# Optimization experiments

Measured on AMD Instinct MI355X. Metric: run time of the kernel, lower is better.

## Reference

```python
import jax, jax.numpy as jnp
import numpy as np

D_MODEL = 1024
HIDDEN = 2048
D_STATE = 16
KERN = 3
BATCH = 2
SEQ = 2048


def _layernorm(x, g, b, eps=1e-5):
    m = jnp.mean(x, axis=-1, keepdims=True)
    v = jnp.var(x, axis=-1, keepdims=True)
    return (x - m) * jax.lax.rsqrt(v + eps) * g + b


def setup_inputs() -> dict:
    key = jax.random.key(0)
    ks = jax.random.split(key, 10)
    w_scale = 0.02  # keep pre-activations in a sane range (mimics trained-net init)
    return {
        "x": jax.random.normal(ks[0], (BATCH, SEQ, D_MODEL), jnp.float32),
        "W_x": jax.random.normal(ks[1], (HIDDEN, D_MODEL), jnp.float32) * w_scale,
        "b_x": jnp.zeros((HIDDEN,), jnp.float32),
        "W_g": jax.random.normal(ks[2], (HIDDEN, D_MODEL), jnp.float32) * w_scale,
        "b_g": jnp.zeros((HIDDEN,), jnp.float32),
        "conv_w": jax.random.normal(ks[3], (HIDDEN, 1, KERN), jnp.float32) * 0.3,
        "conv_b": jnp.zeros((HIDDEN,), jnp.float32),
        "A_raw": jax.random.normal(ks[4], (HIDDEN, D_STATE), jnp.float32),
        "B_ssm": jax.random.normal(ks[5], (HIDDEN, D_STATE), jnp.float32),
        "C_ssm": jax.random.normal(ks[6], (HIDDEN, D_STATE), jnp.float32),
        "W_dt": jax.random.normal(ks[7], (HIDDEN, D_MODEL), jnp.float32) * w_scale,
        "b_dt": jnp.zeros((HIDDEN,), jnp.float32),
        "W_out": jax.random.normal(ks[8], (D_MODEL, HIDDEN), jnp.float32) * w_scale,
        "b_out": jnp.zeros((D_MODEL,), jnp.float32),
        "ln_g": jnp.ones((D_MODEL,), jnp.float32),
        "ln_b": jnp.zeros((D_MODEL,), jnp.float32),
    }


def reference(x, W_x, b_x, W_g, b_g, conv_w, conv_b, A_raw, B_ssm, C_ssm,
              W_dt, b_dt, W_out, b_out, ln_g, ln_b):
    # projections: u, gate
    u = jnp.einsum('bld,hd->blh', x, W_x) + b_x                    # [B,L,H]
    g = jax.nn.sigmoid(jnp.einsum('bld,hd->blh', x, W_g) + b_g)    # [B,L,H]
    # depthwise conv over time (padding = kernel//2, 'same' for odd kernel)
    pad = conv_w.shape[-1] // 2
    h = jax.lax.conv_general_dilated(
        jnp.transpose(u, (0, 2, 1)), conv_w,
        window_strides=(1,), padding=[(pad, pad)],
        feature_group_count=conv_w.shape[0],
        dimension_numbers=('NCH', 'OIH', 'NCH')) + conv_b[None, :, None]
    h = jnp.transpose(h, (0, 2, 1))                                # [B,L,H]
    u = u * g + h * (1.0 - g)
    # time-invariant dt per channel (mean over batch & time, clamped)
    dt = jax.nn.softplus(jnp.einsum('bld,hd->blh', x, W_dt) + b_dt).mean(axis=(0, 1))
    dt = jnp.clip(dt, 1e-3, 2.0)                                   # [H]
    # discretize
    A = -jax.nn.softplus(A_raw)                                    # [H,S]
    A_d = jnp.exp(A * dt[:, None])                                 # [H,S]
    B_d = (A_d - 1.0) / (A + 1e-6) * B_ssm                         # [H,S]
    # selective scan: state s[b,h,k] = A_d*s + B_d*u_t ; y = <s, C>
    Bsz, L, H = u.shape
    S = A_d.shape[1]

    def step(carry, u_t):                                          # u_t: [B,H]
        new = A_d[None] * carry + B_d[None] * u_t[:, :, None]      # [B,H,S]
        y_t = jnp.einsum('bhs,hs->bh', new, C_ssm)
        return new, y_t

    init = jnp.zeros((Bsz, H, S), dtype=u.dtype)
    _, ys = jax.lax.scan(step, init, jnp.transpose(u, (1, 0, 2)))  # ys: [L,B,H]
    y = jnp.transpose(ys, (1, 0, 2))                               # [B,L,H]
    out = jnp.einsum('blh,dh->bld', y, W_out) + b_out
    return _layernorm(x + out, ln_g, ln_b)
```

## Files before the change

kernel.cpp:

```cpp
#include <hip/hip_runtime.h>
#include <math.h>

#define D_MODEL 1024
#define HIDDEN  2048
#define D_STATE 16
#define BATCH   2
#define SEQ     2048
#define NTOK    (BATCH*SEQ)
#define CHUNK   64
#define NCHUNK  (SEQ/CHUNK)

typedef __attribute__((ext_vector_type(8))) short bf16x8;
typedef __attribute__((ext_vector_type(8))) unsigned short ushort8;
typedef __attribute__((ext_vector_type(4))) float f32x4;

#define GLOAD_LDS16(gptr, lptr) \
    __builtin_amdgcn_global_load_lds((const __attribute__((address_space(1))) void*)(gptr), \
                                     (__attribute__((address_space(3))) void*)(lptr), 16, 0, 0)

__device__ __forceinline__ float softplus_f(float x) {
    return fmaxf(x, 0.0f) + log1pf(expf(-fabsf(x)));
}
__device__ __forceinline__ float sigmoid_f(float x) {
    return 1.0f / (1.0f + expf(-x));
}
__device__ __forceinline__ ushort f2bf(float f) {
    unsigned u = __float_as_uint(f);
    unsigned r = (u + 0x7fffu + ((u >> 16) & 1u)) >> 16;
    return (ushort)r;
}
__device__ __forceinline__ float bf2f(ushort u) {
    return __uint_as_float(((unsigned)u) << 16);
}

__global__ __launch_bounds__(256) void cvt_all(
    const float* __restrict__ x, const float* __restrict__ Wx,
    const float* __restrict__ Wg, const float* __restrict__ Wdt,
    const float* __restrict__ Wout, ushort* __restrict__ arena)
{
    int i = blockIdx.x * 256 + threadIdx.x;
    const float* src; int base;
    if      (i < 1048576) { src = x;    base = 0; }
    else if (i < 1572864) { src = Wx;   base = 1048576; }
    else if (i < 2097152) { src = Wg;   base = 1572864; }
    else if (i < 2621440) { src = Wdt;  base = 2097152; }
    else                  { src = Wout; base = 2621440; }
    float4 v = reinterpret_cast<const float4*>(src)[i - base];
    ushort4 o = { f2bf(v.x), f2bf(v.y), f2bf(v.z), f2bf(v.w) };
    reinterpret_cast<ushort4*>(arena)[i] = o;
}

__device__ __forceinline__ void kloop_pipe3(
    const ushort* __restrict__ A, const ushort* __restrict__ B,
    int K, int m0, int n0, ushort* As, ushort* Bs,
    f32x4 (&acc)[4][4], int lane, int w, int wm, int wn)
{
    const int lr   = lane >> 2;
    const int qsrc = (lane & 3) ^ ((lane >> 3) & 3);
    const int kc   = qsrc * 8;
    const int quad = lane >> 4;
    const int fr   = lane & 15;
    const int chq  = quad ^ ((fr >> 1) & 3);

    const int slab0 = w * 2;
    const int r0 = slab0 * 16 + lr;
    const int r1 = r0 + 16;
    const size_t ga0 = (size_t)(m0 + r0) * K + kc;
    const size_t ga1 = (size_t)(m0 + r1) * K + kc;
    const size_t gb0 = (size_t)(n0 + r0) * K + kc;
    const size_t gb1 = (size_t)(n0 + r1) * K + kc;

    const int niter = K / 32;
    GLOAD_LDS16(A + ga0,      &As[slab0 * 512]);
    GLOAD_LDS16(A + ga1,      &As[slab0 * 512 + 512]);
    GLOAD_LDS16(B + gb0,      &Bs[slab0 * 512]);
    GLOAD_LDS16(B + gb1,      &Bs[slab0 * 512 + 512]);
    GLOAD_LDS16(A + ga0 + 32, &As[4096 + slab0 * 512]);
    GLOAD_LDS16(A + ga1 + 32, &As[4096 + slab0 * 512 + 512]);
    GLOAD_LDS16(B + gb0 + 32, &Bs[4096 + slab0 * 512]);
    GLOAD_LDS16(B + gb1 + 32, &Bs[4096 + slab0 * 512 + 512]);

    int buf = 0;
    for (int i = 0; i < niter; i++) {
        asm volatile("s_waitcnt vmcnt(4) lgkmcnt(0)" ::: "memory");
        asm volatile("s_barrier" ::: "memory");
        int nb = buf + 2; if (nb >= 3) nb -= 3;
        const size_t koff = (i + 2 < niter) ? (size_t)(i + 2) * 32 : 0;
        GLOAD_LDS16(A + ga0 + koff, &As[nb * 4096 + slab0 * 512]);
        GLOAD_LDS16(A + ga1 + koff, &As[nb * 4096 + slab0 * 512 + 512]);
        GLOAD_LDS16(B + gb0 + koff, &Bs[nb * 4096 + slab0 * 512]);
        GLOAD_LDS16(B + gb1 + koff, &Bs[nb * 4096 + slab0 * 512 + 512]);

        const ushort* as = &As[buf * 4096];
        const ushort* bs = &Bs[buf * 4096];
        bf16x8 af[4], bfv[4];
        #pragma unroll
        for (int t = 0; t < 4; t++) {
            af[t]  = *reinterpret_cast<const bf16x8*>(&as[(wm * 64 + t * 16 + fr) * 32 + chq * 8]);
            bfv[t] = *reinterpret_cast<const bf16x8*>(&bs[(wn * 64 + t * 16 + fr) * 32 + chq * 8]);
        }
        #pragma unroll
        for (int ii = 0; ii < 4; ii++)
            #pragma unroll
            for (int jj = 0; jj < 4; jj++)
                acc[ii][jj] = __builtin_amdgcn_mfma_f32_16x16x32_bf16(af[ii], bfv[jj], acc[ii][jj], 0, 0, 0);
        buf = (buf == 2) ? 0 : buf + 1;
    }
    asm volatile("s_waitcnt vmcnt(0) lgkmcnt(0)" ::: "memory");
    asm volatile("s_barrier" ::: "memory");
}

__global__ __launch_bounds__(256) void proj_gemm_fused(
    const ushort* __restrict__ xbf, const ushort* __restrict__ Wcat,
    const float* __restrict__ b_x, const float* __restrict__ b_g,
    const float* __restrict__ b_dt, ushort* __restrict__ u_out,
    ushort* __restrict__ g_out, float* __restrict__ dt_sum)
{
    __shared__ ushort S[24576];
    ushort* As = S;
    ushort* Bs = S + 12288;
    const int tid = threadIdx.x, lane = tid & 63, w = tid >> 6;
    const int wm = w & 1, wn = w >> 1;
    const int m0 = blockIdx.x * 128, n0 = blockIdx.y * 128;
    const int quad = lane >> 4, fr = lane & 15;

    f32x4 acc[4][4];
    #pragma unroll
    for (int i = 0; i < 4; i++)
        #pragma unroll
        for (int j = 0; j < 4; j++)
            acc[i][j] = (f32x4){0.f, 0.f, 0.f, 0.f};

    kloop_pipe3(xbf, Wcat, D_MODEL, m0, n0, As, Bs, acc, lane, w, wm, wn);

    const int region = n0 >> 11;
    const int ncb = n0 & 2047;

    if (region == 2) {
        #pragma unroll
        for (int j = 0; j < 4; j++) {
            int n = ncb + wn * 64 + j * 16 + fr;
            float bj = b_dt[n];
            float s = 0.f;
            #pragma unroll
            for (int i = 0; i < 4; i++)
                #pragma unroll
                for (int r = 0; r < 4; r++)
                    s += softplus_f(acc[i][j][r] + bj);
            s += __shfl_xor(s, 16);
            s += __shfl_xor(s, 32);
            if (lane < 16) atomicAdd(&dt_sum[n], s);
        }
    } else {
        const float* bias = region ? b_g : b_x;
        ushort* out = region ? g_out : u_out;
        ushort* Cs = S;
        #pragma unroll
        for (int j = 0; j < 4; j++) {
            int col = wn * 64 + j * 16 + fr;
            float bj = bias[ncb + col];
            #pragma unroll
            for (int i = 0; i < 4; i++) {
                int row = wm * 64 + i * 16 + quad * 4;
                #pragma unroll
                for (int r = 0; r < 4; r++) {
                    float v = acc[i][j][r] + bj;
                    if (region) v = sigmoid_f(v);
                    Cs[(row + r) * 128 + col] = f2bf(v);
                }
            }
        }
        __syncthreads();
        #pragma unroll
        for (int k = 0; k < 8; k++) {
            int v = k * 256 + tid;
            int row = v >> 4, c = (v & 15) * 8;
            *reinterpret_cast<ushort8*>(&out[(size_t)(m0 + row) * HIDDEN + ncb + c]) =
                *reinterpret_cast<const ushort8*>(&Cs[v * 8]);
        }
    }
}

__global__ __launch_bounds__(256) void gemm_out64(
    const ushort* __restrict__ ybf, const ushort* __restrict__ Wout,
    const float* __restrict__ b_out, const float* __restrict__ x,
    float* __restrict__ resid)
{
    __shared__ ushort S[18432];
    ushort* As = S;
    ushort* Bs = S + 6144;
    const int tid = threadIdx.x, lane = tid & 63, w = tid >> 6;
    const int m0 = blockIdx.x * 64, n0 = blockIdx.y * 128;
    const int quad = lane >> 4, fr = lane & 15;
    const int lr   = lane >> 2;
    const int qsrc = (lane & 3) ^ ((lane >> 3) & 3);
    const int chq  = quad ^ ((fr >> 1) & 3);
    const int K = HIDDEN;

    const size_t ga  = (size_t)(m0 + w * 16 + lr) * K + qsrc * 8;
    const size_t gb0 = (size_t)(n0 + w * 16 + lr) * K + qsrc * 8;
    const size_t gb1 = gb0 + (size_t)64 * K;

    f32x4 acc[4][2];
    #pragma unroll
    for (int i = 0; i < 4; i++)
        #pragma unroll
        for (int j = 0; j < 2; j++)
            acc[i][j] = (f32x4){0.f, 0.f, 0.f, 0.f};

    GLOAD_LDS16(ybf  + ga,       &As[0 * 2048 + w * 512]);
    GLOAD_LDS16(Wout + gb0,      &Bs[0 * 4096 + w * 512]);
    GLOAD_LDS16(Wout + gb1,      &Bs[0 * 4096 + 2048 + w * 512]);
    GLOAD_LDS16(ybf  + ga + 32,  &As[1 * 2048 + w * 512]);
    GLOAD_LDS16(Wout + gb0 + 32, &Bs[1 * 4096 + w * 512]);
    GLOAD_LDS16(Wout + gb1 + 32, &Bs[1 * 4096 + 2048 + w * 512]);

    int buf = 0;
    for (int t = 0; t < 64; t++) {
        asm volatile("s_waitcnt vmcnt(3) lgkmcnt(0)" ::: "memory");
        asm volatile("s_barrier" ::: "memory");
        int nb = buf + 2; if (nb >= 3) nb -= 3;
        const size_t koff = (t + 2 < 64) ? (size_t)(t + 2) * 32 : 0;
        GLOAD_LDS16(ybf  + ga + koff,  &As[nb * 2048 + w * 512]);
        GLOAD_LDS16(Wout + gb0 + koff, &Bs[nb * 4096 + w * 512]);
        GLOAD_LDS16(Wout + gb1 + koff, &Bs[nb * 4096 + 2048 + w * 512]);

        const ushort* as = &As[buf * 2048];
        const ushort* bs = &Bs[buf * 4096];
        bf16x8 af[4], bfv[2];
        #pragma unroll
        for (int mi = 0; mi < 4; mi++)
            af[mi] = *reinterpret_cast<const bf16x8*>(&as[(mi * 16 + fr) * 32 + chq * 8]);
        #pragma unroll
        for (int nj = 0; nj < 2; nj++)
            bfv[nj] = *reinterpret_cast<const bf16x8*>(&bs[(w * 32 + nj * 16 + fr) * 32 + chq * 8]);
        #pragma unroll
        for (int mi = 0; mi < 4; mi++)
            #pragma unroll
            for (int nj = 0; nj < 2; nj++)
                acc[mi][nj] = __builtin_amdgcn_mfma_f32_16x16x32_bf16(af[mi], bfv[nj], acc[mi][nj], 0, 0, 0);
        buf = (buf == 2) ? 0 : buf + 1;
    }
    asm volatile("s_waitcnt vmcnt(0) lgkmcnt(0)" ::: "memory");
    asm volatile("s_barrier" ::: "memory");

    float* Sf = (float*)S;
    #pragma unroll
    for (int nj = 0; nj < 2; nj++) {
        int col = w * 32 + nj * 16 + fr;
        float bj = b_out[n0 + col];
        #pragma unroll
        for (int mi = 0; mi < 4; mi++) {
            int row = mi * 16 + quad * 4;
            #pragma unroll
            for (int r = 0; r < 4; r++)
                Sf[(row + r) * 128 + col] = acc[mi][nj][r] + bj;
        }
    }
    __syncthreads();
    #pragma unroll
    for (int k = 0; k < 8; k++) {
        int v = k * 256 + tid;
        int row = v >> 5, c = (v & 31) * 4;
        size_t off = (size_t)(m0 + row) * D_MODEL + n0 + c;
        float4 xa = *reinterpret_cast<const float4*>(&x[off]);
        float4 cv = *reinterpret_cast<const float4*>(&Sf[v * 4]);
        float4 o = { cv.x + xa.x, cv.y + xa.y, cv.z + xa.z, cv.w + xa.w };
        *reinterpret_cast<float4*>(&resid[off]) = o;
    }
}

__global__ __launch_bounds__(256) void dt_finalize(
    const float* __restrict__ dt_sum, const float* __restrict__ A_raw,
    const float* __restrict__ B_ssm, float* __restrict__ A_d,
    float* __restrict__ B_d, float* __restrict__ A_dL)
{
    int i = blockIdx.x * 256 + threadIdx.x;
    if (i >= HIDDEN * D_STATE) return;
    int h = i >> 4;
    float dt = dt_sum[h] * (1.0f / NTOK);
    dt = fminf(fmaxf(dt, 1e-3f), 2.0f);
    float Av = -softplus_f(A_raw[i]);
    float Ad = expf(Av * dt);
    float Bd = (Ad - 1.0f) / (Av + 1e-6f) * B_ssm[i];
    A_d[i] = Ad;
    B_d[i] = Bd;
    A_dL[i] = expf(Av * dt * CHUNK);
}

__global__ __launch_bounds__(256) void scan_pass1(
    const ushort* __restrict__ u_bf, const ushort* __restrict__ g_bf,
    const float* __restrict__ conv_w, const float* __restrict__ conv_b,
    const float* __restrict__ A_d, const float* __restrict__ B_d,
    const float* __restrict__ C_ssm,
    ushort* __restrict__ ypart, float* __restrict__ states)
{
    int idx = blockIdx.x * 256 + threadIdx.x;
    int h  = idx & (HIDDEN - 1);
    int bc = idx >> 11;
    int c  = bc & (NCHUNK - 1);
    int b  = bc >> 5;
    float Ad[D_STATE], Bd[D_STATE], Cv[D_STATE], st[D_STATE];
    const float4* a4 = reinterpret_cast<const float4*>(A_d  + h * D_STATE);
    const float4* b4 = reinterpret_cast<const float4*>(B_d  + h * D_STATE);
    const float4* c4 = reinterpret_cast<const float4*>(C_ssm + h * D_STATE);
    #pragma unroll
    for (int q = 0; q < 4; q++) {
        float4 av = a4[q], bv = b4[q], cv = c4[q];
        Ad[q*4+0]=av.x; Ad[q*4+1]=av.y; Ad[q*4+2]=av.z; Ad[q*4+3]=av.w;
        Bd[q*4+0]=bv.x; Bd[q*4+1]=bv.y; Bd[q*4+2]=bv.z; Bd[q*4+3]=bv.w;
        Cv[q*4+0]=cv.x; Cv[q*4+1]=cv.y; Cv[q*4+2]=cv.z; Cv[q*4+3]=cv.w;
    }
    #pragma unroll
    for (int s = 0; s < D_STATE; s++) st[s] = 0.f;

    float w0 = conv_w[h * 3 + 0], w1 = conv_w[h * 3 + 1];
    float w2 = conv_w[h * 3 + 2], cb = conv_b[h];
    const int tok0 = c * CHUNK;
    const size_t base = ((size_t)b * SEQ + tok0) * HIDDEN + h;
    float u_prev = (tok0 > 0) ? bf2f(u_bf[base - HIDDEN]) : 0.f;
    float u_cur  = bf2f(u_bf[base]);
    for (int l = 0; l < CHUNK; l++) {
        float u_next = (tok0 + l + 1 < SEQ) ? bf2f(u_bf[base + (size_t)(l + 1) * HIDDEN]) : 0.f;
        float gv = bf2f(g_bf[base + (size_t)l * HIDDEN]);
        float conv = u_prev * w0 + u_cur * w1 + u_next * w2 + cb;
        float uv = u_cur * gv + conv * (1.0f - gv);
        float y0 = 0.f, y1 = 0.f, y2 = 0.f, y3 = 0.f;
        #pragma unroll
        for (int s = 0; s < D_STATE; s += 4) {
            st[s+0] = fmaf(Ad[s+0], st[s+0], Bd[s+0] * uv);
            st[s+1] = fmaf(Ad[s+1], st[s+1], Bd[s+1] * uv);
            st[s+2] = fmaf(Ad[s+2], st[s+2], Bd[s+2] * uv);
            st[s+3] = fmaf(Ad[s+3], st[s+3], Bd[s+3] * uv);
            y0 = fmaf(st[s+0], Cv[s+0], y0);
            y1 = fmaf(st[s+1], Cv[s+1], y1);
            y2 = fmaf(st[s+2], Cv[s+2], y2);
            y3 = fmaf(st[s+3], Cv[s+3], y3);
        }
        ypart[base + (size_t)l * HIDDEN] = f2bf((y0 + y1) + (y2 + y3));
        u_prev = u_cur; u_cur = u_next;
    }
    float4* sp = reinterpret_cast<float4*>(states + ((size_t)bc * HIDDEN + h) * D_STATE);
    #pragma unroll
    for (int q = 0; q < 4; q++)
        sp[q] = (float4){st[q*4+0], st[q*4+1], st[q*4+2], st[q*4+3]};
}

__global__ __launch_bounds__(256) void scan_pass2(
    float* __restrict__ states, const float* __restrict__ A_dL)
{
    int idx = blockIdx.x * 256 + threadIdx.x;
    int s = idx & 15;
    int h = (idx >> 4) & (HIDDEN - 1);
    int b = idx >> 15;
    float aL = A_dL[h * D_STATE + s];
    float carry = 0.f;
    for (int c = 0; c < NCHUNK; c++) {
        size_t addr = (((size_t)(b * NCHUNK + c) * HIDDEN) + h) * D_STATE + s;
        float fin = states[addr];
        states[addr] = carry;
        carry = fmaf(aL, carry, fin);
    }
}

__global__ __launch_bounds__(256) void scan_pass3(
    const ushort* __restrict__ ypart, const float* __restrict__ states,
    const float* __restrict__ A_d, const float* __restrict__ C_ssm,
    ushort* __restrict__ ybf)
{
    int idx = blockIdx.x * 256 + threadIdx.x;
    int h  = idx & (HIDDEN - 1);
    int bc = idx >> 11;
    int c  = bc & (NCHUNK - 1);
    int b  = bc >> 5;
    float Ad[D_STATE], t[D_STATE];
    const float* sp = states + ((size_t)bc * HIDDEN + h) * D_STATE;
    #pragma unroll
    for (int s = 0; s < D_STATE; s++) {
        float a = A_d[h * D_STATE + s];
        Ad[s] = a;
        t[s] = C_ssm[h * D_STATE + s] * a * sp[s];
    }
    const size_t base = ((size_t)b * SEQ + (size_t)c * CHUNK) * HIDDEN + h;
    for (int l = 0; l < CHUNK; l++) {
        float c0 = 0.f, c1 = 0.f;
        #pragma unroll
        for (int s = 0; s < D_STATE; s += 2) {
            c0 += t[s];
            c1 += t[s + 1];
            t[s] *= Ad[s];
            t[s + 1] *= Ad[s + 1];
        }
        ybf[base + (size_t)l * HIDDEN] = f2bf(bf2f(ypart[base + (size_t)l * HIDDEN]) + (c0 + c1));
    }
}

__global__ __launch_bounds__(256) void ln_kernel(
    const float* __restrict__ resid, const float* __restrict__ ln_g,
    const float* __restrict__ ln_b, float* __restrict__ out)
{
    int row = blockIdx.x;
    int tid = threadIdx.x;
    const float4 v = reinterpret_cast<const float4*>(resid + (size_t)row * D_MODEL)[tid];
    float s  = v.x + v.y + v.z + v.w;
    float ss = v.x * v.x + v.y * v.y + v.z * v.z + v.w * v.w;
    #pragma unroll
    for (int off = 32; off > 0; off >>= 1) {
        s  += __shfl_down(s, off);
        ss += __shfl_down(ss, off);
    }
    __shared__ float sbuf[4], ssbuf[4];
    int wid = tid >> 6, lane = tid & 63;
    if (lane == 0) { sbuf[wid] = s; ssbuf[wid] = ss; }
    __syncthreads();
    float tot  = sbuf[0] + sbuf[1] + sbuf[2] + sbuf[3];
    float tot2 = ssbuf[0] + ssbuf[1] + ssbuf[2] + ssbuf[3];
    float mean = tot * (1.0f / D_MODEL);
    float var  = tot2 * (1.0f / D_MODEL) - mean * mean;
    float rstd = rsqrtf(var + 1e-5f);
    const float4 gv = reinterpret_cast<const float4*>(ln_g)[tid];
    const float4 bv = reinterpret_cast<const float4*>(ln_b)[tid];
    float4 o;
    o.x = (v.x - mean) * rstd * gv.x + bv.x;
    o.y = (v.y - mean) * rstd * gv.y + bv.y;
    o.z = (v.z - mean) * rstd * gv.z + bv.z;
    o.w = (v.w - mean) * rstd * gv.w + bv.w;
    reinterpret_cast<float4*>(out + (size_t)row * D_MODEL)[tid] = o;
}

extern "C" void kernel_launch(void* const* d_in, const int* in_sizes, int n_in,
                              void* d_out, int out_size, void* d_ws, size_t ws_size,
                              hipStream_t stream) {
    const float* x      = (const float*)d_in[0];
    const float* W_x    = (const float*)d_in[1];
    const float* b_x    = (const float*)d_in[2];
    const float* W_g    = (const float*)d_in[3];
    const float* b_g    = (const float*)d_in[4];
    const float* conv_w = (const float*)d_in[5];
    const float* conv_b = (const float*)d_in[6];
    const float* A_raw  = (const float*)d_in[7];
    const float* B_ssm  = (const float*)d_in[8];
    const float* C_ssm  = (const float*)d_in[9];
    const float* W_dt   = (const float*)d_in[10];
    const float* b_dt   = (const float*)d_in[11];
    const float* W_out  = (const float*)d_in[12];
    const float* b_out  = (const float*)d_in[13];
    const float* ln_g   = (const float*)d_in[14];
    const float* ln_b   = (const float*)d_in[15];

    char* W = (char*)d_ws;
    ushort* arena   = (ushort*)(W);
    ushort* x_bf    = arena;
    ushort* Wcat    = arena + 4194304;
    ushort* Wout_bf = arena + 10485760;
    ushort* u_bf    = (ushort*)(W + (24ull << 20));
    ushort* g_bf    = (ushort*)(W + (40ull << 20));
    ushort* ypart   = (ushort*)(W + (56ull << 20));
    float*  resid   = (float*)(W + (40ull << 20));
    float*  states  = (float*)(W + (72ull << 20));
    float*  dt_sum  = (float*)(W + (80ull << 20));
    float*  A_d     = (float*)(W + (80ull << 20) + 65536);
    float*  B_d     = (float*)(W + (80ull << 20) + 65536 + 131072);
    float*  A_dL    = (float*)(W + (80ull << 20) + 65536 + 262144);
    ushort* y_bf    = u_bf;

    hipMemsetAsync(dt_sum, 0, HIDDEN * sizeof(float), stream);

    dim3 blk(256);
    cvt_all<<<12288, blk, 0, stream>>>(x, W_x, W_g, W_dt, W_out, arena);

    dim3 grid_proj(NTOK / 128, 3 * HIDDEN / 128);
    proj_gemm_fused<<<grid_proj, blk, 0, stream>>>(x_bf, Wcat, b_x, b_g, b_dt,
                                                   u_bf, g_bf, dt_sum);
    dt_finalize<<<(HIDDEN * D_STATE) / 256, blk, 0, stream>>>(dt_sum, A_raw, B_ssm,
                                                              A_d, B_d, A_dL);
    scan_pass1<<<(BATCH * NCHUNK * HIDDEN) / 256, blk, 0, stream>>>(
        u_bf, g_bf, conv_w, conv_b, A_d, B_d, C_ssm, ypart, states);
    scan_pass2<<<(BATCH * HIDDEN * D_STATE) / 256, blk, 0, stream>>>(states, A_dL);
    scan_pass3<<<(BATCH * NCHUNK * HIDDEN) / 256, blk, 0, stream>>>(ypart, states, A_d,
                                                                    C_ssm, y_bf);
    dim3 grid_out(NTOK / 64, D_MODEL / 128);
    gemm_out64<<<grid_out, blk, 0, stream>>>(y_bf, Wout_bf, b_out, x, resid);
    ln_kernel<<<NTOK, blk, 0, stream>>>(resid, ln_g, ln_b, (float*)d_out);
}
```

Baseline: 297.5 us.

## Halve scan chunk length and deepen output GEMM K-tile to 64

The scan chunk size drops from 64 to 32 tokens. This doubles the number of independent threads in scan_pass1 and scan_pass3 and shortens each thread's serial loop, at the cost of a longer sequential carry pass and twice the chunk-state storage. To fit that larger buffer, the chunk-state array now reuses the start of the workspace, which is no longer needed by the time the scan runs. The output-projection GEMM moves from 32- to 64-wide K tiles with an 8-way XOR swizzle, halving the number of barrier and wait iterations at the cost of doubling the LDS footprint per block.

```diff
diff --git a/kernel.cpp b/kernel.cpp
--- a/kernel.cpp
+++ b/kernel.cpp
@@ -7,7 +7,7 @@
 #define BATCH   2
 #define SEQ     2048
 #define NTOK    (BATCH*SEQ)
-#define CHUNK   64
+#define CHUNK   32
 #define NCHUNK  (SEQ/CHUNK)
 
 typedef __attribute__((ext_vector_type(8))) short bf16x8;
@@ -186,20 +186,18 @@
     const float* __restrict__ b_out, const float* __restrict__ x,
     float* __restrict__ resid)
 {
-    __shared__ ushort S[18432];
+    __shared__ ushort S[36864];
     ushort* As = S;
-    ushort* Bs = S + 6144;
+    ushort* Bs = S + 12288;
     const int tid = threadIdx.x, lane = tid & 63, w = tid >> 6;
     const int m0 = blockIdx.x * 64, n0 = blockIdx.y * 128;
     const int quad = lane >> 4, fr = lane & 15;
-    const int lr   = lane >> 2;
-    const int qsrc = (lane & 3) ^ ((lane >> 3) & 3);
-    const int chq  = quad ^ ((fr >> 1) & 3);
+    const int lr8  = lane >> 3;
+    const int q8   = (lane & 7) ^ (lr8 & 7);
     const int K = HIDDEN;
 
-    const size_t ga  = (size_t)(m0 + w * 16 + lr) * K + qsrc * 8;
-    const size_t gb0 = (size_t)(n0 + w * 16 + lr) * K + qsrc * 8;
-    const size_t gb1 = gb0 + (size_t)64 * K;
+    const size_t ga = (size_t)(m0 + w * 16 + lr8) * K + q8 * 8;
+    const size_t gb = (size_t)(n0 + w * 32 + lr8) * K + q8 * 8;
 
     f32x4 acc[4][2];
     #pragma unroll
@@ -208,41 +206,50 @@
         for (int j = 0; j < 2; j++)
             acc[i][j] = (f32x4){0.f, 0.f, 0.f, 0.f};
 
-    GLOAD_LDS16(ybf  + ga,       &As[0 * 2048 + w * 512]);
-    GLOAD_LDS16(Wout + gb0,      &Bs[0 * 4096 + w * 512]);
-    GLOAD_LDS16(Wout + gb1,      &Bs[0 * 4096 + 2048 + w * 512]);
-    GLOAD_LDS16(ybf  + ga + 32,  &As[1 * 2048 + w * 512]);
-    GLOAD_LDS16(Wout + gb0 + 32, &Bs[1 * 4096 + w * 512]);
-    GLOAD_LDS16(Wout + gb1 + 32, &Bs[1 * 4096 + 2048 + w * 512]);
+#define STAGE_OUT(KT, BUF) do {                                                   \
+    const size_t ko_ = (size_t)(KT) * 64;                                         \
+    GLOAD_LDS16(ybf  + ga + ko_,            &As[(BUF)*4096 + (w*2+0)*512]);       \
+    GLOAD_LDS16(ybf  + ga + 8*K + ko_,      &As[(BUF)*4096 + (w*2+1)*512]);       \
+    GLOAD_LDS16(Wout + gb + ko_,            &Bs[(BUF)*8192 + (w*4+0)*512]);       \
+    GLOAD_LDS16(Wout + gb + 8*K + ko_,      &Bs[(BUF)*8192 + (w*4+1)*512]);       \
+    GLOAD_LDS16(Wout + gb + 16*K + ko_,     &Bs[(BUF)*8192 + (w*4+2)*512]);       \
+    GLOAD_LDS16(Wout + gb + 24*K + ko_,     &Bs[(BUF)*8192 + (w*4+3)*512]);       \
+  } while (0)
+
+    STAGE_OUT(0, 0);
+    STAGE_OUT(1, 1);
 
     int buf = 0;
-    for (int t = 0; t < 64; t++) {
-        asm volatile("s_waitcnt vmcnt(3) lgkmcnt(0)" ::: "memory");
+    for (int t = 0; t < 32; t++) {
+        asm volatile("s_waitcnt vmcnt(6) lgkmcnt(0)" ::: "memory");
         asm volatile("s_barrier" ::: "memory");
         int nb = buf + 2; if (nb >= 3) nb -= 3;
-        const size_t koff = (t + 2 < 64) ? (size_t)(t + 2) * 32 : 0;
-        GLOAD_LDS16(ybf  + ga + koff,  &As[nb * 2048 + w * 512]);
-        GLOAD_LDS16(Wout + gb0 + koff, &Bs[nb * 4096 + w * 512]);
-        GLOAD_LDS16(Wout + gb1 + koff, &Bs[nb * 4096 + 2048 + w * 512]);
-
-        const ushort* as = &As[buf * 2048];
-        const ushort* bs = &Bs[buf * 4096];
-        bf16x8 af[4], bfv[2];
-        #pragma unroll
-        for (int mi = 0; mi < 4; mi++)
-            af[mi] = *reinterpret_cast<const bf16x8*>(&as[(mi * 16 + fr) * 32 + chq * 8]);
-        #pragma unroll
-        for (int nj = 0; nj < 2; nj++)
-            bfv[nj] = *reinterpret_cast<const bf16x8*>(&bs[(w * 32 + nj * 16 + fr) * 32 + chq * 8]);
-        #pragma unroll
-        for (int mi = 0; mi < 4; mi++)
+        const int kt = (t + 2 < 32) ? (t + 2) : 0;
+        STAGE_OUT(kt, nb);
+
+        const ushort* as = &As[buf * 4096];
+        const ushort* bs = &Bs[buf * 8192];
+        #pragma unroll
+        for (int ks = 0; ks < 2; ks++) {
+            const int ch = ((ks * 4 + quad) ^ (fr & 7)) * 8;
+            bf16x8 af[4], bfv[2];
+            #pragma unroll
+            for (int mi = 0; mi < 4; mi++)
+                af[mi] = *reinterpret_cast<const bf16x8*>(&as[(mi * 16 + fr) * 64 + ch]);
             #pragma unroll
             for (int nj = 0; nj < 2; nj++)
-                acc[mi][nj] = __builtin_amdgcn_mfma_f32_16x16x32_bf16(af[mi], bfv[nj], acc[mi][nj], 0, 0, 0);
+                bfv[nj] = *reinterpret_cast<const bf16x8*>(&bs[(w * 32 + nj * 16 + fr) * 64 + ch]);
+            #pragma unroll
+            for (int mi = 0; mi < 4; mi++)
+                #pragma unroll
+                for (int nj = 0; nj < 2; nj++)
+                    acc[mi][nj] = __builtin_amdgcn_mfma_f32_16x16x32_bf16(af[mi], bfv[nj], acc[mi][nj], 0, 0, 0);
+        }
         buf = (buf == 2) ? 0 : buf + 1;
     }
     asm volatile("s_waitcnt vmcnt(0) lgkmcnt(0)" ::: "memory");
     asm volatile("s_barrier" ::: "memory");
+#undef STAGE_OUT
 
     float* Sf = (float*)S;
     #pragma unroll
@@ -299,7 +306,7 @@
     int h  = idx & (HIDDEN - 1);
     int bc = idx >> 11;
     int c  = bc & (NCHUNK - 1);
-    int b  = bc >> 5;
+    int b  = bc / NCHUNK;
     float Ad[D_STATE], Bd[D_STATE], Cv[D_STATE], st[D_STATE];
     const float4* a4 = reinterpret_cast<const float4*>(A_d  + h * D_STATE);
     const float4* b4 = reinterpret_cast<const float4*>(B_d  + h * D_STATE);
@@ -372,7 +379,7 @@
     int h  = idx & (HIDDEN - 1);
     int bc = idx >> 11;
     int c  = bc & (NCHUNK - 1);
-    int b  = bc >> 5;
+    int b  = bc / NCHUNK;
     float Ad[D_STATE], t[D_STATE];
     const float* sp = states + ((size_t)bc * HIDDEN + h) * D_STATE;
     #pragma unroll
@@ -457,7 +464,7 @@
     ushort* g_bf    = (ushort*)(W + (40ull << 20));
     ushort* ypart   = (ushort*)(W + (56ull << 20));
     float*  resid   = (float*)(W + (40ull << 20));
-    float*  states  = (float*)(W + (72ull << 20));
+    float*  states  = (float*)(W);
     float*  dt_sum  = (float*)(W + (80ull << 20));
     float*  A_d     = (float*)(W + (80ull << 20) + 65536);
     float*  B_d     = (float*)(W + (80ull << 20) + 65536 + 131072);
```

Measured after the change: 288.2 us. 1.03x faster.
